# Kernel tuning notes

Hardware: AMD Instinct MI355X
Metric: run time of the kernel (lower is better)

Reference implementation:

```python
import jax, jax.numpy as jnp
import numpy as np

B, D, T, DEPTH, O = 65536, 1024, 64, 1, 2


def setup_inputs() -> dict:
    key = jax.random.key(0)
    k1, k2, k3 = jax.random.split(key, 3)
    x = jax.random.normal(k1, (B, D), dtype=jnp.float32)
    feature_selectors = jax.random.normal(k2, (T, DEPTH, D), dtype=jnp.float32)
    thresholds = jnp.zeros((T, DEPTH), dtype=jnp.float32)
    leaf_weights = jax.random.normal(k3, (T, 2 ** DEPTH, O), dtype=jnp.float32)
    return {"x": x, "feature_selectors": feature_selectors,
            "thresholds": thresholds, "leaf_weights": leaf_weights}


def reference(x, feature_selectors, thresholds, leaf_weights):
    # Batched over all trees at once (original loops per-tree).
    # logits: [B, T, depth]
    logits = jnp.einsum('bd,tkd->btk', x, feature_selectors) - thresholds[None]
    p = jax.nn.sigmoid(logits)
    # stack([p, 1-p], -1): [B, T, depth, 2]; prod over depth axis -> [B, T, 2]
    leaf_probs = jnp.prod(jnp.stack([p, 1.0 - p], axis=-1), axis=2)
    # per-tree leaf_probs @ weights, summed over trees -> [B, O]
    return jnp.einsum('btk,tko->bo', leaf_probs, leaf_weights)
```

## Files before the change

kernel.cpp:

```cpp
#include <hip/hip_runtime.h>
#include <hip/hip_bf16.h>

#define NB    65536
#define ND    1024
#define NT    64
#define BK    64
#define NCH   (ND / BK)
#define ROWS  64

typedef __attribute__((ext_vector_type(8))) short bf16x8;
typedef __attribute__((ext_vector_type(4))) short bf16x4;
typedef __attribute__((ext_vector_type(4))) float f32x4;

__device__ __forceinline__ short f2bf_s(float f) {
    __hip_bfloat16 h = __float2bfloat16(f);
    return __builtin_bit_cast(short, h);
}

__device__ __forceinline__ void phase_barrier() {
    asm volatile("s_waitcnt lgkmcnt(0)\n\ts_barrier" ::: "memory");
}

__global__ __launch_bounds__(256, 4) void node_main(const float* __restrict__ x,
                                                    const float* __restrict__ F,
                                                    const float* __restrict__ thr,
                                                    const float* __restrict__ lw,
                                                    float* __restrict__ out) {
    __shared__ __align__(16) __hip_bfloat16 Abuf[2][ROWS * BK];

    const int tid  = threadIdx.x;
    const int w    = tid >> 6;
    const int lane = tid & 63;
    const int c    = lane & 15;
    const int g    = lane >> 4;
    const int rot  = blockIdx.x & (NCH - 1);
    const long blockRow = (long)blockIdx.x * ROWS;
    const float* xbase = x + blockRow * ND;

    const int srow = tid >> 4;
    const int scol = tid & 15;

    const int   t     = w * 16 + c;
    const float thr_t = thr[t];
    const float w00 = lw[t * 4 + 0], w01 = lw[t * 4 + 1];
    const float w10 = lw[t * 4 + 2], w11 = lw[t * 4 + 3];
    const float* Ffrow = F + (long)t * ND;

    f32x4 acc[4];
#pragma unroll
    for (int rt = 0; rt < 4; ++rt) acc[rt] = (f32x4){0.f, 0.f, 0.f, 0.f};

    f32x4  rA0[4], rA1[4];
    bf16x8 rB0[2], rB1[2];

    auto chmap = [&](int ch) { return (ch + rot) & (NCH - 1); };

    auto load_chunk = [&](int ch, f32x4* rA) {
        const int cm = chmap(ch);
#pragma unroll
        for (int i = 0; i < 4; ++i) {
            const int r = i * 16 + srow;
            rA[i] = *(const f32x4*)(xbase + (long)r * ND + cm * BK + scol * 4);
        }
    };
    auto loadB = [&](int ch, bf16x8* rB) {
        const int cm = chmap(ch);
#pragma unroll
        for (int kk = 0; kk < 2; ++kk) {
            const float* fp = Ffrow + cm * BK + kk * 32 + g * 8;
            f32x4 b0 = *(const f32x4*)(fp);
            f32x4 b1 = *(const f32x4*)(fp + 4);
            bf16x8 bf;
            bf[0] = f2bf_s(b0[0]); bf[1] = f2bf_s(b0[1]);
            bf[2] = f2bf_s(b0[2]); bf[3] = f2bf_s(b0[3]);
            bf[4] = f2bf_s(b1[0]); bf[5] = f2bf_s(b1[1]);
            bf[6] = f2bf_s(b1[2]); bf[7] = f2bf_s(b1[3]);
            rB[kk] = bf;
        }
    };
    auto stage_write = [&](int buf, const f32x4* rA) {
#pragma unroll
        for (int i = 0; i < 4; ++i) {
            const int r = i * 16 + srow;
            f32x4 a = rA[i];
            bf16x4 v;
            v[0] = f2bf_s(a[0]); v[1] = f2bf_s(a[1]);
            v[2] = f2bf_s(a[2]); v[3] = f2bf_s(a[3]);
            const int s = (scol >> 1) ^ (r & 7);
            char* p = (char*)(&Abuf[buf][0]) + r * 128 + (s << 4) + ((scol & 1) << 3);
            *(bf16x4*)p = v;
        }
    };
    auto compute = [&](int buf, const bf16x8* rB) {
#pragma unroll
        for (int kk = 0; kk < 2; ++kk) {
#pragma unroll
            for (int rt = 0; rt < 4; ++rt) {
                const int r    = rt * 16 + c;
                const int slot = (kk * 4 + g) ^ (r & 7);
                bf16x8 afrag = *(const bf16x8*)(&Abuf[buf][r * BK + slot * 8]);
                acc[rt] = __builtin_amdgcn_mfma_f32_16x16x32_bf16(afrag, rB[kk], acc[rt], 0, 0, 0);
            }
        }
    };

    load_chunk(0, rA0);
    load_chunk(1, rA1);
    loadB(0, rB0);
    loadB(1, rB1);
    stage_write(0, rA0);
    phase_barrier();

#pragma unroll
    for (int ch2 = 0; ch2 < NCH; ch2 += 2) {
        if (ch2 + 2 < NCH) load_chunk(ch2 + 2, rA0);
        compute(0, rB0);
        if (ch2 + 2 < NCH) loadB(ch2 + 2, rB0);
        stage_write(1, rA1);
        phase_barrier();
        if (ch2 + 3 < NCH) load_chunk(ch2 + 3, rA1);
        compute(1, rB1);
        if (ch2 + 3 < NCH) loadB(ch2 + 3, rB1);
        if (ch2 + 2 < NCH) stage_write(0, rA0);
        phase_barrier();
    }

    float* partials = (float*)(&Abuf[0][0]);
#pragma unroll
    for (int rt = 0; rt < 4; ++rt) {
#pragma unroll
        for (int reg = 0; reg < 4; ++reg) {
            const float logit = acc[rt][reg] - thr_t;
            const float p = 1.0f / (1.0f + __expf(-logit));
            float o0 = w10 + p * (w00 - w10);
            float o1 = w11 + p * (w01 - w11);
#pragma unroll
            for (int m = 1; m < 16; m <<= 1) {
                o0 += __shfl_xor(o0, m, 64);
                o1 += __shfl_xor(o1, m, 64);
            }
            if (c == 0) {
                const int row = rt * 16 + g * 4 + reg;
                partials[(w * ROWS + row) * 2 + 0] = o0;
                partials[(w * ROWS + row) * 2 + 1] = o1;
            }
        }
    }
    __syncthreads();
    if (tid < 128) {
        const int row = tid >> 1, o = tid & 1;
        const float s = partials[(0 * ROWS + row) * 2 + o] + partials[(1 * ROWS + row) * 2 + o] +
                        partials[(2 * ROWS + row) * 2 + o] + partials[(3 * ROWS + row) * 2 + o];
        out[(blockRow + row) * 2 + o] = s;
    }
}

extern "C" void kernel_launch(void* const* d_in, const int* in_sizes, int n_in,
                              void* d_out, int out_size, void* d_ws, size_t ws_size,
                              hipStream_t stream) {
    const float* x   = (const float*)d_in[0];
    const float* fs  = (const float*)d_in[1];
    const float* thr = (const float*)d_in[2];
    const float* lw  = (const float*)d_in[3];
    float* out = (float*)d_out;
    (void)in_sizes; (void)n_in; (void)out_size; (void)d_ws; (void)ws_size;

    node_main<<<NB / ROWS, 256, 0, stream>>>(x, fs, thr, lw, out);
}
```

Measured before the change: 49.29 us.

## Double K-chunk width and restructure register prefetch pipeline

Raises the K-chunk size from 64 to 128. This halves the number of chunks and barriers and doubles the MFMA work done per barrier. The two A register buffers are replaced by a single 8-entry buffer, and the loop is rewritten as a single-step software pipeline: compute the current LDS buffer, stage the next chunk, then issue global loads two chunks ahead. The catch is that global loads now issue after the stage-write rather than before compute, which may reduce latency hiding. The larger LDS footprint (32 KB) may also lower occupancy.

```diff
diff --git a/kernel.cpp b/kernel.cpp
--- a/kernel.cpp
+++ b/kernel.cpp
@@ -4,7 +4,7 @@
 #define NB    65536
 #define ND    1024
 #define NT    64
-#define BK    64
+#define BK    128
 #define NCH   (ND / BK)
 #define ROWS  64
 
@@ -50,23 +50,25 @@
 #pragma unroll
     for (int rt = 0; rt < 4; ++rt) acc[rt] = (f32x4){0.f, 0.f, 0.f, 0.f};
 
-    f32x4  rA0[4], rA1[4];
-    bf16x8 rB0[2], rB1[2];
+    f32x4  rA[8];
+    bf16x8 rB0[4], rB1[4];
 
     auto chmap = [&](int ch) { return (ch + rot) & (NCH - 1); };
 
-    auto load_chunk = [&](int ch, f32x4* rA) {
+    auto load_chunk = [&](int ch) {
         const int cm = chmap(ch);
 #pragma unroll
-        for (int i = 0; i < 4; ++i) {
-            const int r = i * 16 + srow;
-            rA[i] = *(const f32x4*)(xbase + (long)r * ND + cm * BK + scol * 4);
-        }
+        for (int i = 0; i < 4; ++i)
+#pragma unroll
+            for (int h = 0; h < 2; ++h) {
+                const int r = i * 16 + srow;
+                rA[i * 2 + h] = *(const f32x4*)(xbase + (long)r * ND + cm * BK + (scol + 16 * h) * 4);
+            }
     };
     auto loadB = [&](int ch, bf16x8* rB) {
         const int cm = chmap(ch);
 #pragma unroll
-        for (int kk = 0; kk < 2; ++kk) {
+        for (int kk = 0; kk < 4; ++kk) {
             const float* fp = Ffrow + cm * BK + kk * 32 + g * 8;
             f32x4 b0 = *(const f32x4*)(fp);
             f32x4 b1 = *(const f32x4*)(fp + 4);
@@ -78,50 +80,51 @@
             rB[kk] = bf;
         }
     };
-    auto stage_write = [&](int buf, const f32x4* rA) {
+    auto stage_write = [&](int buf) {
 #pragma unroll
-        for (int i = 0; i < 4; ++i) {
-            const int r = i * 16 + srow;
-            f32x4 a = rA[i];
-            bf16x4 v;
-            v[0] = f2bf_s(a[0]); v[1] = f2bf_s(a[1]);
-            v[2] = f2bf_s(a[2]); v[3] = f2bf_s(a[3]);
-            const int s = (scol >> 1) ^ (r & 7);
-            char* p = (char*)(&Abuf[buf][0]) + r * 128 + (s << 4) + ((scol & 1) << 3);
-            *(bf16x4*)p = v;
-        }
+        for (int i = 0; i < 4; ++i)
+#pragma unroll
+            for (int h = 0; h < 2; ++h) {
+                const int r  = i * 16 + srow;
+                const int g8 = scol + 16 * h;
+                f32x4 a = rA[i * 2 + h];
+                bf16x4 v;
+                v[0] = f2bf_s(a[0]); v[1] = f2bf_s(a[1]);
+                v[2] = f2bf_s(a[2]); v[3] = f2bf_s(a[3]);
+                const int slot = (g8 >> 1) ^ (r & 7);
+                char* p = (char*)(&Abuf[buf][0]) + r * 256 + (slot << 4) + ((g8 & 1) << 3);
+                *(bf16x4*)p = v;
+            }
     };
     auto compute = [&](int buf, const bf16x8* rB) {
 #pragma unroll
-        for (int kk = 0; kk < 2; ++kk) {
+        for (int kk = 0; kk < 4; ++kk) {
 #pragma unroll
             for (int rt = 0; rt < 4; ++rt) {
                 const int r    = rt * 16 + c;
                 const int slot = (kk * 4 + g) ^ (r & 7);
-                bf16x8 afrag = *(const bf16x8*)(&Abuf[buf][r * BK + slot * 8]);
+                bf16x8 afrag = *(const bf16x8*)((const char*)(&Abuf[buf][0]) + r * 256 + (slot << 4));
                 acc[rt] = __builtin_amdgcn_mfma_f32_16x16x32_bf16(afrag, rB[kk], acc[rt], 0, 0, 0);
             }
         }
     };
 
-    load_chunk(0, rA0);
-    load_chunk(1, rA1);
+    load_chunk(0);
     loadB(0, rB0);
+    stage_write(0);
+    load_chunk(1);
     loadB(1, rB1);
-    stage_write(0, rA0);
     phase_barrier();
 
 #pragma unroll
-    for (int ch2 = 0; ch2 < NCH; ch2 += 2) {
-        if (ch2 + 2 < NCH) load_chunk(ch2 + 2, rA0);
-        compute(0, rB0);
-        if (ch2 + 2 < NCH) loadB(ch2 + 2, rB0);
-        stage_write(1, rA1);
-        phase_barrier();
-        if (ch2 + 3 < NCH) load_chunk(ch2 + 3, rA1);
-        compute(1, rB1);
-        if (ch2 + 3 < NCH) loadB(ch2 + 3, rB1);
-        if (ch2 + 2 < NCH) stage_write(0, rA0);
+    for (int p = 0; p < NCH; ++p) {
+        const int cur = p & 1;
+        compute(cur, cur ? rB1 : rB0);
+        if (p + 1 < NCH) stage_write(cur ^ 1);
+        if (p + 2 < NCH) {
+            load_chunk(p + 2);
+            loadB(p + 2, cur ? rB1 : rB0);
+        }
         phase_barrier();
     }
 
```

Result: slower. 56.08 us (+13.8%).
